# Optimization experiments

Hardware: AMD Instinct MI355X
Metric: run time of the kernel (lower is better)

Reference implementation:

```python
import jax, jax.numpy as jnp
import numpy as np

B, N, DIN, H, A = 4096, 32, 256, 128, 32  # batch, n_agents, din, hidden_dim, n_actions
NEG = 9e15


def _linear_params(key, fan_in, fan_out):
    kw, kb = jax.random.split(key)
    bound = 1.0 / np.sqrt(fan_in)
    w = jax.random.uniform(kw, (fan_in, fan_out), jnp.float32, -bound, bound)
    b = jax.random.uniform(kb, (fan_out,), jnp.float32, -bound, bound)
    return w, b


def setup_inputs() -> dict:
    key = jax.random.key(0)
    ks = jax.random.split(key, 12)
    x = jax.random.normal(ks[0], (B, N, DIN), jnp.float32)
    mask = jax.random.randint(ks[1], (B, N, N), 0, 2).astype(jnp.float32)
    enc_w, enc_b = _linear_params(ks[2], DIN, H)
    a1_vw, a1_vb = _linear_params(ks[3], H, H)
    a1_kw, a1_kb = _linear_params(ks[4], H, H)
    a1_qw, a1_qb = _linear_params(ks[5], H, H)
    a1_ow, a1_ob = _linear_params(ks[6], H, H)
    a2_vw, a2_vb = _linear_params(ks[7], H, H)
    a2_kw, a2_kb = _linear_params(ks[8], H, H)
    a2_qw, a2_qb = _linear_params(ks[9], H, H)
    a2_ow, a2_ob = _linear_params(ks[10], H, H)
    q_w, q_b = _linear_params(ks[11], H, A)
    return dict(x=x, mask=mask, enc_w=enc_w, enc_b=enc_b,
                a1_vw=a1_vw, a1_vb=a1_vb, a1_kw=a1_kw, a1_kb=a1_kb,
                a1_qw=a1_qw, a1_qb=a1_qb, a1_ow=a1_ow, a1_ob=a1_ob,
                a2_vw=a2_vw, a2_vb=a2_vb, a2_kw=a2_kw, a2_kb=a2_kb,
                a2_qw=a2_qw, a2_qb=a2_qb, a2_ow=a2_ow, a2_ob=a2_ob,
                q_w=q_w, q_b=q_b)


def _att_block(h, mask, vw, vb, kw, kb, qw, qb, ow, ob):
    # h: [B, N, H]; mask: [B, N, N]
    v = jax.nn.relu(jnp.einsum('bnd,dh->bnh', h, vw) + vb)
    q = jax.nn.relu(jnp.einsum('bnd,dh->bnh', h, qw) + qb)
    k = jax.nn.relu(jnp.einsum('bnd,dh->bnh', h, kw) + kb)
    scores = jnp.einsum('bih,bjh->bij', q, k)               # [B, N, N]
    logits = scores * mask - NEG * (1.0 - mask)
    att = jax.nn.softmax(logits, axis=2)
    out = jnp.einsum('bij,bjh->bih', att, v)
    return jax.nn.relu(jnp.einsum('bnh,ho->bno', out, ow) + ob)


def reference(x, mask, enc_w, enc_b,
              a1_vw, a1_vb, a1_kw, a1_kb, a1_qw, a1_qb, a1_ow, a1_ob,
              a2_vw, a2_vb, a2_kw, a2_kb, a2_qw, a2_qb, a2_ow, a2_ob,
              q_w, q_b):
    h1 = jax.nn.relu(jnp.einsum('bnd,dh->bnh', x, enc_w) + enc_b)
    h2 = _att_block(h1, mask, a1_vw, a1_vb, a1_kw, a1_kb, a1_qw, a1_qb, a1_ow, a1_ob)
    h3 = _att_block(h2, mask, a2_vw, a2_vb, a2_kw, a2_kb, a2_qw, a2_qb, a2_ow, a2_ob)
    q = jnp.einsum('bnh,ha->bna', h3, q_w) + q_b            # [B, N, A]
    return q
```

## Files before the change

kernel.cpp:

```cpp
#include <hip/hip_runtime.h>
#include <hip/hip_bf16.h>

typedef __attribute__((ext_vector_type(8))) short bf16x8;
typedef __attribute__((ext_vector_type(4))) short bf16x4;
typedef __attribute__((ext_vector_type(4))) float f32x4;

#define DEVI static __device__ __forceinline__

constexpr int NAG = 32, DIN = 256, HDIM = 128, ADIM = 32;
constexpr int G = 2;

constexpr int WS_ENC = 0;
constexpr int WS_H   = 32768;
constexpr int WS_QW  = 32768 + 8 * 16384;
constexpr int WS_TOT = WS_QW + 4096;

DEVI short f2bf(float f) {
  union { float f; unsigned u; } a; a.f = f;
  unsigned r = (a.u + 0x7fffu + ((a.u >> 16) & 1u)) >> 16;
  return (short)r;
}

__global__ void prep_weights(const float* __restrict__ enc_w,
                             const float* __restrict__ m0, const float* __restrict__ m1,
                             const float* __restrict__ m2, const float* __restrict__ m3,
                             const float* __restrict__ m4, const float* __restrict__ m5,
                             const float* __restrict__ m6, const float* __restrict__ m7,
                             const float* __restrict__ qw,
                             short* __restrict__ ws)
{
  const int i = blockIdx.x * 256 + threadIdx.x;
  if (i >= WS_TOT) return;
  const float* src; int Nout, e, base, sh, ntm;
  if (i < 32768) { src = enc_w; Nout = 128; e = i; base = 0; sh = 3; ntm = 7; }
  else if (i < WS_QW) {
    const int m = (i - 32768) >> 14;
    e = (i - 32768) & 16383; base = 32768 + (m << 14);
    const float* tab[8] = {m0, m1, m2, m3, m4, m5, m6, m7};
    src = tab[m]; Nout = 128; sh = 3; ntm = 7;
  } else { src = qw; Nout = 32; e = i - WS_QW; base = WS_QW; sh = 1; ntm = 1; }
  const int j = e & 7, lane = (e >> 3) & 63, tile = e >> 9;
  const int nt = tile & ntm, ks = tile >> sh;
  const int row = ks * 32 + (lane >> 4) * 8 + j;
  const int col = nt * 16 + (lane & 15);
  ws[base + e] = f2bf(src[row * Nout + col]);
}

template<int KSTEPS, bool RELU, bool TRANS>
DEVI void linearWG(const short* __restrict__ src, int sstride,
                   const short* __restrict__ wfrag, const float* __restrict__ bias,
                   short* __restrict__ dst, int dstride,
                   int wave, int lr, int lq)
{
  f32x4 acc[4][2];
#pragma unroll
  for (int mt = 0; mt < 4; ++mt)
#pragma unroll
    for (int t = 0; t < 2; ++t) acc[mt][t] = (f32x4){0.f, 0.f, 0.f, 0.f};

  const int lane = lq * 16 + lr;
  bf16x8 bf[KSTEPS][2];
  const bf16x8* wp = (const bf16x8*)wfrag;
#pragma unroll
  for (int ks = 0; ks < KSTEPS; ++ks)
#pragma unroll
    for (int t = 0; t < 2; ++t)
      bf[ks][t] = wp[(ks * 8 + wave * 2 + t) * 64 + lane];

#pragma unroll
  for (int ks = 0; ks < KSTEPS; ++ks) {
    bf16x8 af[4];
#pragma unroll
    for (int mt = 0; mt < 4; ++mt)
      af[mt] = *(const bf16x8*)(src + (mt * 16 + lr) * sstride + ks * 32 + lq * 8);
#pragma unroll
    for (int mt = 0; mt < 4; ++mt)
#pragma unroll
      for (int t = 0; t < 2; ++t)
        acc[mt][t] = __builtin_amdgcn_mfma_f32_16x16x32_bf16(af[mt], bf[ks][t], acc[mt][t], 0, 0, 0);
  }

#pragma unroll
  for (int t = 0; t < 2; ++t) {
    const int col = wave * 32 + t * 16 + lr;
    const float bv = bias[col];
#pragma unroll
    for (int mt = 0; mt < 4; ++mt) {
      if (!TRANS) {
#pragma unroll
        for (int r = 0; r < 4; ++r) {
          const int row = mt * 16 + lq * 4 + r;
          float v = acc[mt][t][r] + bv;
          if (RELU) v = fmaxf(v, 0.f);
          dst[row * dstride + col] = f2bf(v);
        }
      } else {
        bf16x4 s;
#pragma unroll
        for (int r = 0; r < 4; ++r) {
          float v = acc[mt][t][r] + bv;
          if (RELU) v = fmaxf(v, 0.f);
          s[r] = f2bf(v);
        }
        *(bf16x4*)(dst + col * dstride + mt * 16 + lq * 4) = s;
      }
    }
  }
}

DEVI void att_block(short* HB, short* AB, short* BB, short* AT, float* ST,
                    const short* wv, const short* wk, const short* wq, const short* wo,
                    const float* bv, const float* bk, const float* bq, const float* bo,
                    const float* __restrict__ mask, int b0,
                    int wave, int lr, int lq)
{
  linearWG<4, true, false>(HB, 136, wq, bq, AB, 136, wave, lr, lq);
  linearWG<4, true, false>(HB, 136, wk, bk, BB, 136, wave, lr, lq);
  __syncthreads();

  const int g = wave >> 1, half = wave & 1;
  float lg[2][4];
  {
    f32x4 sacc[2];
    sacc[0] = (f32x4){0, 0, 0, 0}; sacc[1] = (f32x4){0, 0, 0, 0};
#pragma unroll
    for (int ks = 0; ks < 4; ++ks) {
      const bf16x8 kf = *(const bf16x8*)(BB + (g * 32 + half * 16 + lr) * 136 + ks * 32 + lq * 8);
#pragma unroll
      for (int mt = 0; mt < 2; ++mt) {
        const bf16x8 qf = *(const bf16x8*)(AB + (g * 32 + mt * 16 + lr) * 136 + ks * 32 + lq * 8);
        sacc[mt] = __builtin_amdgcn_mfma_f32_16x16x32_bf16(qf, kf, sacc[mt], 0, 0, 0);
      }
    }
    const float* mp = mask + (size_t)(b0 + g) * (NAG * NAG);
    float mx[2][4], sm[2][4];
#pragma unroll
    for (int mt = 0; mt < 2; ++mt)
#pragma unroll
      for (int r = 0; r < 4; ++r) {
        const int row = mt * 16 + lq * 4 + r, col = half * 16 + lr;
        const float m = mp[row * 32 + col];
        const float l = sacc[mt][r] * m - 9e15f * (1.f - m);
        lg[mt][r] = l;
        float v = l;
        v = fmaxf(v, __shfl_xor(v, 1)); v = fmaxf(v, __shfl_xor(v, 2));
        v = fmaxf(v, __shfl_xor(v, 4)); v = fmaxf(v, __shfl_xor(v, 8));
        mx[mt][r] = v;
        float e = __expf(l - v);
        e += __shfl_xor(e, 1); e += __shfl_xor(e, 2);
        e += __shfl_xor(e, 4); e += __shfl_xor(e, 8);
        sm[mt][r] = e;
      }
    if (lr == 0) {
#pragma unroll
      for (int mt = 0; mt < 2; ++mt)
#pragma unroll
        for (int r = 0; r < 4; ++r) {
          const int row = g * 32 + mt * 16 + lq * 4 + r;
          float2 p; p.x = mx[mt][r]; p.y = sm[mt][r];
          *(float2*)(ST + row * 4 + half * 2) = p;
        }
    }
  }
  __syncthreads();
  {
#pragma unroll
    for (int mt = 0; mt < 2; ++mt)
#pragma unroll
      for (int r = 0; r < 4; ++r) {
        const int row = g * 32 + mt * 16 + lq * 4 + r, col = half * 16 + lr;
        const float4 s4 = *(const float4*)(ST + row * 4);
        const float M = fmaxf(s4.x, s4.z);
        const float T = s4.y * __expf(s4.x - M) + s4.w * __expf(s4.z - M);
        const float a = __expf(lg[mt][r] - M) / T;
        AT[row * 40 + col] = f2bf(a);
      }
  }
  __syncthreads();

  linearWG<4, true, true>(HB, 136, wv, bv, BB, 72, wave, lr, lq);
  __syncthreads();

  {
    f32x4 acc[2][4];
#pragma unroll
    for (int mt = 0; mt < 2; ++mt)
#pragma unroll
      for (int nt = 0; nt < 4; ++nt) acc[mt][nt] = (f32x4){0, 0, 0, 0};
    bf16x8 pa[2];
#pragma unroll
    for (int mt = 0; mt < 2; ++mt)
      pa[mt] = *(const bf16x8*)(AT + (g * 32 + mt * 16 + lr) * 40 + lq * 8);
#pragma unroll
    for (int nt = 0; nt < 4; ++nt) {
      const bf16x8 vf = *(const bf16x8*)(BB + (half * 64 + nt * 16 + lr) * 72 + g * 32 + lq * 8);
#pragma unroll
      for (int mt = 0; mt < 2; ++mt)
        acc[mt][nt] = __builtin_amdgcn_mfma_f32_16x16x32_bf16(pa[mt], vf, acc[mt][nt], 0, 0, 0);
    }
#pragma unroll
    for (int nt = 0; nt < 4; ++nt)
#pragma unroll
      for (int mt = 0; mt < 2; ++mt)
#pragma unroll
        for (int r = 0; r < 4; ++r) {
          const int row = g * 32 + mt * 16 + lq * 4 + r;
          const int col = half * 64 + nt * 16 + lr;
          AB[row * 136 + col] = f2bf(acc[mt][nt][r]);
        }
  }
  __syncthreads();

  linearWG<4, true, false>(AB, 136, wo, bo, HB, 136, wave, lr, lq);
  __syncthreads();
}

__global__ __launch_bounds__(256, 2)
void dgn_main(const float* __restrict__ x, const float* __restrict__ mask,
              const float* __restrict__ enc_b,
              const float* __restrict__ b1v, const float* __restrict__ b1k,
              const float* __restrict__ b1q, const float* __restrict__ b1o,
              const float* __restrict__ b2v, const float* __restrict__ b2k,
              const float* __restrict__ b2q, const float* __restrict__ b2o,
              const float* __restrict__ qb,
              const short* __restrict__ wf,
              float* __restrict__ out)
{
  __shared__ __align__(16) char smem[59392];
  short* HB = (short*)(smem);
  short* AB = (short*)(smem + 17408);
  short* BB = (short*)(smem + 34816);
  short* AT = (short*)(smem + 53248);
  float* ST = (float*)(smem + 58368);
  short* XB = (short*)(smem + 17408);

  const int tid = threadIdx.x;
  const int wave = tid >> 6, lane = tid & 63;
  const int lr = lane & 15, lq = lane >> 4;
  const int b0 = blockIdx.x * G;

  {
    const float4* xsrc = (const float4*)(x + (size_t)b0 * NAG * DIN);
#pragma unroll
    for (int it = 0; it < 16; ++it) {
      const int q4 = tid + it * 256;
      const float4 v = xsrc[q4];
      const int row = q4 >> 6;
      const int col = (q4 & 63) * 4;
      bf16x4 s;
      s[0] = f2bf(v.x); s[1] = f2bf(v.y); s[2] = f2bf(v.z); s[3] = f2bf(v.w);
      *(bf16x4*)(XB + row * 264 + col) = s;
    }
  }
  __syncthreads();

  linearWG<8, true, false>(XB, 264, wf + WS_ENC, enc_b, HB, 136, wave, lr, lq);
  __syncthreads();

  att_block(HB, AB, BB, AT, ST,
            wf + WS_H + 0 * 16384, wf + WS_H + 1 * 16384,
            wf + WS_H + 2 * 16384, wf + WS_H + 3 * 16384,
            b1v, b1k, b1q, b1o, mask, b0, wave, lr, lq);

  att_block(HB, AB, BB, AT, ST,
            wf + WS_H + 4 * 16384, wf + WS_H + 5 * 16384,
            wf + WS_H + 6 * 16384, wf + WS_H + 7 * 16384,
            b2v, b2k, b2q, b2o, mask, b0, wave, lr, lq);

  {
    f32x4 facc[2];
    facc[0] = (f32x4){0, 0, 0, 0}; facc[1] = (f32x4){0, 0, 0, 0};
    const bf16x8* wq = (const bf16x8*)(wf + WS_QW);
    bf16x8 bq[4][2];
#pragma unroll
    for (int ks = 0; ks < 4; ++ks)
#pragma unroll
      for (int t = 0; t < 2; ++t)
        bq[ks][t] = wq[(ks * 2 + t) * 64 + lane];
#pragma unroll
    for (int ks = 0; ks < 4; ++ks) {
      const bf16x8 af = *(const bf16x8*)(HB + (wave * 16 + lr) * 136 + ks * 32 + lq * 8);
      facc[0] = __builtin_amdgcn_mfma_f32_16x16x32_bf16(af, bq[ks][0], facc[0], 0, 0, 0);
      facc[1] = __builtin_amdgcn_mfma_f32_16x16x32_bf16(af, bq[ks][1], facc[1], 0, 0, 0);
    }
#pragma unroll
    for (int t = 0; t < 2; ++t) {
      const int col = t * 16 + lr;
      const float bvv = qb[col];
#pragma unroll
      for (int r = 0; r < 4; ++r) {
        const int row = wave * 16 + lq * 4 + r;
        const int g = row >> 5, ag = row & 31;
        out[(((size_t)(b0 + g) * NAG) + ag) * ADIM + col] = facc[t][r] + bvv;
      }
    }
  }
}

extern "C" void kernel_launch(void* const* d_in, const int* in_sizes, int n_in,
                              void* d_out, int out_size, void* d_ws, size_t ws_size,
                              hipStream_t stream)
{
  const float* x     = (const float*)d_in[0];
  const float* mask  = (const float*)d_in[1];
  const float* enc_w = (const float*)d_in[2];
  const float* enc_b = (const float*)d_in[3];
  const float* a1_vw = (const float*)d_in[4];
  const float* a1_vb = (const float*)d_in[5];
  const float* a1_kw = (const float*)d_in[6];
  const float* a1_kb = (const float*)d_in[7];
  const float* a1_qw = (const float*)d_in[8];
  const float* a1_qb = (const float*)d_in[9];
  const float* a1_ow = (const float*)d_in[10];
  const float* a1_ob = (const float*)d_in[11];
  const float* a2_vw = (const float*)d_in[12];
  const float* a2_vb = (const float*)d_in[13];
  const float* a2_kw = (const float*)d_in[14];
  const float* a2_kb = (const float*)d_in[15];
  const float* a2_qw = (const float*)d_in[16];
  const float* a2_qb = (const float*)d_in[17];
  const float* a2_ow = (const float*)d_in[18];
  const float* a2_ob = (const float*)d_in[19];
  const float* q_w   = (const float*)d_in[20];
  const float* q_b   = (const float*)d_in[21];
  short* ws = (short*)d_ws;

  prep_weights<<<(WS_TOT + 255) / 256, 256, 0, stream>>>(
      enc_w, a1_vw, a1_kw, a1_qw, a1_ow, a2_vw, a2_kw, a2_qw, a2_ow, q_w, ws);

  dgn_main<<<4096 / G, 256, 0, stream>>>(
      x, mask, enc_b,
      a1_vb, a1_kb, a1_qb, a1_ob,
      a2_vb, a2_kb, a2_qb, a2_ob,
      q_b, ws, (float*)d_out);
}
```

Before: 319.8 us.

## Use 8 waves per block with rotated LDS buffers and weight prefetch

Doubles the block from 4 to 8 waves so each wave computes a 16-column slice of every linear layer. Attention scores, softmax and the att·V product are redistributed across the 8 waves. LDS is reorganized into three rotating buffers so the block uses less shared memory and one barrier per attention block is removed. Weight fragments are now prefetched one k-step ahead instead of all held in registers, cutting register pressure so the launch bounds can target higher occupancy (512 threads, 6). The trade-off is more per-wave loads of the A operand from LDS, since each wave reloads the same rows for fewer output columns.

New measurement: 320.6 us. Within noise of the previous version (+0.3%).

```diff
diff --git a/kernel.cpp b/kernel.cpp
--- a/kernel.cpp
+++ b/kernel.cpp
@@ -14,6 +14,12 @@
 constexpr int WS_H   = 32768;
 constexpr int WS_QW  = 32768 + 8 * 16384;
 constexpr int WS_TOT = WS_QW + 4096;
+
+constexpr int L_R0 = 0;
+constexpr int L_R1 = 17408;
+constexpr int L_R2 = 34816;
+constexpr int L_ST = 53248;
+constexpr int L_TOT = 54272;
 
 DEVI short f2bf(float f) {
   union { float f; unsigned u; } a; a.f = f;
@@ -47,175 +53,146 @@
 }
 
 template<int KSTEPS, bool RELU, bool TRANS>
-DEVI void linearWG(const short* __restrict__ src, int sstride,
-                   const short* __restrict__ wfrag, const float* __restrict__ bias,
-                   short* __restrict__ dst, int dstride,
-                   int wave, int lr, int lq)
-{
-  f32x4 acc[4][2];
-#pragma unroll
-  for (int mt = 0; mt < 4; ++mt)
-#pragma unroll
-    for (int t = 0; t < 2; ++t) acc[mt][t] = (f32x4){0.f, 0.f, 0.f, 0.f};
-
-  const int lane = lq * 16 + lr;
-  bf16x8 bf[KSTEPS][2];
+DEVI void linearW(const short* __restrict__ src, int sstride,
+                  const short* __restrict__ wfrag, const float* __restrict__ bias,
+                  short* __restrict__ dst, int dstride,
+                  int wave, int lr, int lq, int lane)
+{
+  f32x4 acc[4];
+#pragma unroll
+  for (int mt = 0; mt < 4; ++mt) acc[mt] = (f32x4){0.f, 0.f, 0.f, 0.f};
+
   const bf16x8* wp = (const bf16x8*)wfrag;
-#pragma unroll
-  for (int ks = 0; ks < KSTEPS; ++ks)
-#pragma unroll
-    for (int t = 0; t < 2; ++t)
-      bf[ks][t] = wp[(ks * 8 + wave * 2 + t) * 64 + lane];
-
+  bf16x8 bcur = wp[(0 * 8 + wave) * 64 + lane];
 #pragma unroll
   for (int ks = 0; ks < KSTEPS; ++ks) {
+    bf16x8 bnxt = bcur;
+    if (ks + 1 < KSTEPS) bnxt = wp[((ks + 1) * 8 + wave) * 64 + lane];
     bf16x8 af[4];
 #pragma unroll
     for (int mt = 0; mt < 4; ++mt)
       af[mt] = *(const bf16x8*)(src + (mt * 16 + lr) * sstride + ks * 32 + lq * 8);
 #pragma unroll
     for (int mt = 0; mt < 4; ++mt)
-#pragma unroll
-      for (int t = 0; t < 2; ++t)
-        acc[mt][t] = __builtin_amdgcn_mfma_f32_16x16x32_bf16(af[mt], bf[ks][t], acc[mt][t], 0, 0, 0);
-  }
-
-#pragma unroll
-  for (int t = 0; t < 2; ++t) {
-    const int col = wave * 32 + t * 16 + lr;
-    const float bv = bias[col];
-#pragma unroll
-    for (int mt = 0; mt < 4; ++mt) {
-      if (!TRANS) {
-#pragma unroll
-        for (int r = 0; r < 4; ++r) {
-          const int row = mt * 16 + lq * 4 + r;
-          float v = acc[mt][t][r] + bv;
-          if (RELU) v = fmaxf(v, 0.f);
-          dst[row * dstride + col] = f2bf(v);
-        }
-      } else {
-        bf16x4 s;
-#pragma unroll
-        for (int r = 0; r < 4; ++r) {
-          float v = acc[mt][t][r] + bv;
-          if (RELU) v = fmaxf(v, 0.f);
-          s[r] = f2bf(v);
-        }
-        *(bf16x4*)(dst + col * dstride + mt * 16 + lq * 4) = s;
+      acc[mt] = __builtin_amdgcn_mfma_f32_16x16x32_bf16(af[mt], bcur, acc[mt], 0, 0, 0);
+    bcur = bnxt;
+  }
+
+  const int col = wave * 16 + lr;
+  const float bv = bias[col];
+#pragma unroll
+  for (int mt = 0; mt < 4; ++mt) {
+    if (!TRANS) {
+#pragma unroll
+      for (int r = 0; r < 4; ++r) {
+        float v = acc[mt][r] + bv;
+        if (RELU) v = fmaxf(v, 0.f);
+        dst[(mt * 16 + lq * 4 + r) * dstride + col] = f2bf(v);
       }
-    }
-  }
-}
-
-DEVI void att_block(short* HB, short* AB, short* BB, short* AT, float* ST,
+    } else {
+      bf16x4 s;
+#pragma unroll
+      for (int r = 0; r < 4; ++r) {
+        float v = acc[mt][r] + bv;
+        if (RELU) v = fmaxf(v, 0.f);
+        s[r] = f2bf(v);
+      }
+      *(bf16x4*)(dst + col * dstride + mt * 16 + lq * 4) = s;
+    }
+  }
+}
+
+DEVI void att_block(short* Rh, short* Rq, short* R2, float* ST,
                     const short* wv, const short* wk, const short* wq, const short* wo,
                     const float* bv, const float* bk, const float* bq, const float* bo,
                     const float* __restrict__ mask, int b0,
-                    int wave, int lr, int lq)
-{
-  linearWG<4, true, false>(HB, 136, wq, bq, AB, 136, wave, lr, lq);
-  linearWG<4, true, false>(HB, 136, wk, bk, BB, 136, wave, lr, lq);
-  __syncthreads();
-
-  const int g = wave >> 1, half = wave & 1;
-  float lg[2][4];
+                    int wave, int lr, int lq, int lane)
+{
+  linearW<4, true, false>(Rh, 136, wq, bq, Rq, 136, wave, lr, lq, lane);
+  linearW<4, true, false>(Rh, 136, wk, bk, R2, 136, wave, lr, lq, lane);
+  __syncthreads();
+
+  const int g = wave >> 2, smt = (wave >> 1) & 1, snt = wave & 1;
+  float lg[4];
   {
-    f32x4 sacc[2];
-    sacc[0] = (f32x4){0, 0, 0, 0}; sacc[1] = (f32x4){0, 0, 0, 0};
+    f32x4 sacc = (f32x4){0, 0, 0, 0};
 #pragma unroll
     for (int ks = 0; ks < 4; ++ks) {
-      const bf16x8 kf = *(const bf16x8*)(BB + (g * 32 + half * 16 + lr) * 136 + ks * 32 + lq * 8);
-#pragma unroll
-      for (int mt = 0; mt < 2; ++mt) {
-        const bf16x8 qf = *(const bf16x8*)(AB + (g * 32 + mt * 16 + lr) * 136 + ks * 32 + lq * 8);
-        sacc[mt] = __builtin_amdgcn_mfma_f32_16x16x32_bf16(qf, kf, sacc[mt], 0, 0, 0);
+      const bf16x8 qf = *(const bf16x8*)(Rq + (g * 32 + smt * 16 + lr) * 136 + ks * 32 + lq * 8);
+      const bf16x8 kf = *(const bf16x8*)(R2 + (g * 32 + snt * 16 + lr) * 136 + ks * 32 + lq * 8);
+      sacc = __builtin_amdgcn_mfma_f32_16x16x32_bf16(qf, kf, sacc, 0, 0, 0);
+    }
+    const float* mp = mask + (size_t)(b0 + g) * (NAG * NAG);
+#pragma unroll
+    for (int r = 0; r < 4; ++r) {
+      const int row = smt * 16 + lq * 4 + r, col = snt * 16 + lr;
+      const float m = mp[row * 32 + col];
+      const float l = sacc[r] * m - 9e15f * (1.f - m);
+      lg[r] = l;
+      float v = l;
+      v = fmaxf(v, __shfl_xor(v, 1)); v = fmaxf(v, __shfl_xor(v, 2));
+      v = fmaxf(v, __shfl_xor(v, 4)); v = fmaxf(v, __shfl_xor(v, 8));
+      float e = __expf(l - v);
+      e += __shfl_xor(e, 1); e += __shfl_xor(e, 2);
+      e += __shfl_xor(e, 4); e += __shfl_xor(e, 8);
+      if (lr == 0) {
+        float2 p; p.x = v; p.y = e;
+        *(float2*)(ST + (g * 32 + row) * 4 + snt * 2) = p;
       }
     }
-    const float* mp = mask + (size_t)(b0 + g) * (NAG * NAG);
-    float mx[2][4], sm[2][4];
+  }
+  __syncthreads();
+
+  short* AT = Rq;
+#pragma unroll
+  for (int r = 0; r < 4; ++r) {
+    const int row = g * 32 + smt * 16 + lq * 4 + r, col = snt * 16 + lr;
+    const float4 s4 = *(const float4*)(ST + row * 4);
+    const float M = fmaxf(s4.x, s4.z);
+    const float T = s4.y * __expf(s4.x - M) + s4.w * __expf(s4.z - M);
+    const float a = __expf(lg[r] - M) / T;
+    AT[row * 40 + col] = f2bf(a);
+  }
+
+  linearW<4, true, true>(Rh, 136, wv, bv, R2, 72, wave, lr, lq, lane);
+  __syncthreads();
+
+  {
+    const int cq = wave & 3, pg = wave >> 2;
+    f32x4 acc[2][2];
 #pragma unroll
     for (int mt = 0; mt < 2; ++mt)
 #pragma unroll
-      for (int r = 0; r < 4; ++r) {
-        const int row = mt * 16 + lq * 4 + r, col = half * 16 + lr;
-        const float m = mp[row * 32 + col];
-        const float l = sacc[mt][r] * m - 9e15f * (1.f - m);
-        lg[mt][r] = l;
-        float v = l;
-        v = fmaxf(v, __shfl_xor(v, 1)); v = fmaxf(v, __shfl_xor(v, 2));
-        v = fmaxf(v, __shfl_xor(v, 4)); v = fmaxf(v, __shfl_xor(v, 8));
-        mx[mt][r] = v;
-        float e = __expf(l - v);
-        e += __shfl_xor(e, 1); e += __shfl_xor(e, 2);
-        e += __shfl_xor(e, 4); e += __shfl_xor(e, 8);
-        sm[mt][r] = e;
-      }
-    if (lr == 0) {
-#pragma unroll
-      for (int mt = 0; mt < 2; ++mt)
-#pragma unroll
-        for (int r = 0; r < 4; ++r) {
-          const int row = g * 32 + mt * 16 + lq * 4 + r;
-          float2 p; p.x = mx[mt][r]; p.y = sm[mt][r];
-          *(float2*)(ST + row * 4 + half * 2) = p;
-        }
-    }
-  }
-  __syncthreads();
-  {
+      for (int nt = 0; nt < 2; ++nt) acc[mt][nt] = (f32x4){0, 0, 0, 0};
+    bf16x8 pa[2];
 #pragma unroll
     for (int mt = 0; mt < 2; ++mt)
-#pragma unroll
-      for (int r = 0; r < 4; ++r) {
-        const int row = g * 32 + mt * 16 + lq * 4 + r, col = half * 16 + lr;
-        const float4 s4 = *(const float4*)(ST + row * 4);
-        const float M = fmaxf(s4.x, s4.z);
-        const float T = s4.y * __expf(s4.x - M) + s4.w * __expf(s4.z - M);
-        const float a = __expf(lg[mt][r] - M) / T;
-        AT[row * 40 + col] = f2bf(a);
-      }
-  }
-  __syncthreads();
-
-  linearWG<4, true, true>(HB, 136, wv, bv, BB, 72, wave, lr, lq);
-  __syncthreads();
-
-  {
-    f32x4 acc[2][4];
-#pragma unroll
-    for (int mt = 0; mt < 2; ++mt)
-#pragma unroll
-      for (int nt = 0; nt < 4; ++nt) acc[mt][nt] = (f32x4){0, 0, 0, 0};
-    bf16x8 pa[2];
-#pragma unroll
-    for (int mt = 0; mt < 2; ++mt)
-      pa[mt] = *(const bf16x8*)(AT + (g * 32 + mt * 16 + lr) * 40 + lq * 8);
-#pragma unroll
-    for (int nt = 0; nt < 4; ++nt) {
-      const bf16x8 vf = *(const bf16x8*)(BB + (half * 64 + nt * 16 + lr) * 72 + g * 32 + lq * 8);
+      pa[mt] = *(const bf16x8*)(AT + (pg * 32 + mt * 16 + lr) * 40 + lq * 8);
+#pragma unroll
+    for (int nt = 0; nt < 2; ++nt) {
+      const bf16x8 vf = *(const bf16x8*)(R2 + (cq * 32 + nt * 16 + lr) * 72 + pg * 32 + lq * 8);
 #pragma unroll
       for (int mt = 0; mt < 2; ++mt)
         acc[mt][nt] = __builtin_amdgcn_mfma_f32_16x16x32_bf16(pa[mt], vf, acc[mt][nt], 0, 0, 0);
     }
 #pragma unroll
-    for (int nt = 0; nt < 4; ++nt)
+    for (int nt = 0; nt < 2; ++nt)
 #pragma unroll
       for (int mt = 0; mt < 2; ++mt)
 #pragma unroll
         for (int r = 0; r < 4; ++r) {
-          const int row = g * 32 + mt * 16 + lq * 4 + r;
-          const int col = half * 64 + nt * 16 + lr;
-          AB[row * 136 + col] = f2bf(acc[mt][nt][r]);
+          const int row = pg * 32 + mt * 16 + lq * 4 + r;
+          const int col = cq * 32 + nt * 16 + lr;
+          Rh[row * 136 + col] = f2bf(acc[mt][nt][r]);
         }
   }
   __syncthreads();
 
-  linearWG<4, true, false>(AB, 136, wo, bo, HB, 136, wave, lr, lq);
-  __syncthreads();
-}
-
-__global__ __launch_bounds__(256, 2)
+  linearW<4, true, false>(Rh, 136, wo, bo, Rq, 136, wave, lr, lq, lane);
+  __syncthreads();
+}
+
+__global__ __launch_bounds__(512, 6)
 void dgn_main(const float* __restrict__ x, const float* __restrict__ mask,
               const float* __restrict__ enc_b,
               const float* __restrict__ b1v, const float* __restrict__ b1k,
@@ -226,13 +203,12 @@
               const short* __restrict__ wf,
               float* __restrict__ out)
 {
-  __shared__ __align__(16) char smem[59392];
-  short* HB = (short*)(smem);
-  short* AB = (short*)(smem + 17408);
-  short* BB = (short*)(smem + 34816);
-  short* AT = (short*)(smem + 53248);
-  float* ST = (float*)(smem + 58368);
-  short* XB = (short*)(smem + 17408);
+  __shared__ __align__(16) char smem[L_TOT];
+  short* R0 = (short*)(smem + L_R0);
+  short* R1 = (short*)(smem + L_R1);
+  short* R2 = (short*)(smem + L_R2);
+  float* ST = (float*)(smem + L_ST);
+  short* XB = (short*)(smem + L_R1);
 
   const int tid = threadIdx.x;
   const int wave = tid >> 6, lane = tid & 63;
@@ -242,8 +218,8 @@
   {
     const float4* xsrc = (const float4*)(x + (size_t)b0 * NAG * DIN);
 #pragma unroll
-    for (int it = 0; it < 16; ++it) {
-      const int q4 = tid + it * 256;
+    for (int it = 0; it < 8; ++it) {
+      const int q4 = tid + it * 512;
       const float4 v = xsrc[q4];
       const int row = q4 >> 6;
       const int col = (q4 & 63) * 4;
@@ -254,45 +230,39 @@
   }
   __syncthreads();
 
-  linearWG<8, true, false>(XB, 264, wf + WS_ENC, enc_b, HB, 136, wave, lr, lq);
-  __syncthreads();
-
-  att_block(HB, AB, BB, AT, ST,
+  linearW<8, true, false>(XB, 264, wf + WS_ENC, enc_b, R0, 136, wave, lr, lq, lane);
+  __syncthreads();
+
+  att_block(R0, R1, R2, ST,
             wf + WS_H + 0 * 16384, wf + WS_H + 1 * 16384,
             wf + WS_H + 2 * 16384, wf + WS_H + 3 * 16384,
-            b1v, b1k, b1q, b1o, mask, b0, wave, lr, lq);
-
-  att_block(HB, AB, BB, AT, ST,
+            b1v, b1k, b1q, b1o, mask, b0, wave, lr, lq, lane);
+
+  att_block(R1, R0, R2, ST,
             wf + WS_H + 4 * 16384, wf + WS_H + 5 * 16384,
             wf + WS_H + 6 * 16384, wf + WS_H + 7 * 16384,
-            b2v, b2k, b2q, b2o, mask, b0, wave, lr, lq);
+            b2v, b2k, b2q, b2o, mask, b0, wave, lr, lq, lane);
 
   {
-    f32x4 facc[2];
-    facc[0] = (f32x4){0, 0, 0, 0}; facc[1] = (f32x4){0, 0, 0, 0};
-    const bf16x8* wq = (const bf16x8*)(wf + WS_QW);
-    bf16x8 bq[4][2];
+    const int hmt = wave >> 1, ht = wave & 1;
+    f32x4 facc = (f32x4){0, 0, 0, 0};
+    const bf16x8* wp = (const bf16x8*)(wf + WS_QW);
+    bf16x8 bq[4];
 #pragma unroll
     for (int ks = 0; ks < 4; ++ks)
-#pragma unroll
-      for (int t = 0; t < 2; ++t)
-        bq[ks][t] = wq[(ks * 2 + t) * 64 + lane];
+      bq[ks] = wp[(ks * 2 + ht) * 64 + lane];
 #pragma unroll
     for (int ks = 0; ks < 4; ++ks) {
-      const bf16x8 af = *(const bf16x8*)(HB + (wave * 16 + lr) * 136 + ks * 32 + lq * 8);
-      facc[0] = __builtin_amdgcn_mfma_f32_16x16x32_bf16(af, bq[ks][0], facc[0], 0, 0, 0);
-      facc[1] = __builtin_amdgcn_mfma_f32_16x16x32_bf16(af, bq[ks][1], facc[1], 0, 0, 0);
-    }
-#pragma unroll
-    for (int t = 0; t < 2; ++t) {
-      const int col = t * 16 + lr;
-      const float bvv = qb[col];
-#pragma unroll
-      for (int r = 0; r < 4; ++r) {
-        const int row = wave * 16 + lq * 4 + r;
-        const int g = row >> 5, ag = row & 31;
-        out[(((size_t)(b0 + g) * NAG) + ag) * ADIM + col] = facc[t][r] + bvv;
-      }
+      const bf16x8 af = *(const bf16x8*)(R0 + (hmt * 16 + lr) * 136 + ks * 32 + lq * 8);
+      facc = __builtin_amdgcn_mfma_f32_16x16x32_bf16(af, bq[ks], facc, 0, 0, 0);
+    }
+    const int col = ht * 16 + lr;
+    const float bvv = qb[col];
+#pragma unroll
+    for (int r = 0; r < 4; ++r) {
+      const int row = hmt * 16 + lq * 4 + r;
+      const int gg = row >> 5, ag = row & 31;
+      out[(((size_t)(b0 + gg) * NAG) + ag) * ADIM + col] = facc[r] + bvv;
     }
   }
 }
@@ -328,7 +298,7 @@
   prep_weights<<<(WS_TOT + 255) / 256, 256, 0, stream>>>(
       enc_w, a1_vw, a1_kw, a1_qw, a1_ow, a2_vw, a2_kw, a2_qw, a2_ow, q_w, ws);
 
-  dgn_main<<<4096 / G, 256, 0, stream>>>(
+  dgn_main<<<4096 / G, 512, 0, stream>>>(
       x, mask, enc_b,
       a1_vb, a1_kb, a1_qb, a1_ob,
       a2_vb, a2_kb, a2_qb, a2_ob,
```
